# Kernel optimization log

Measured on AMD Instinct MI355X. Metric: run time of the kernel, lower is better.

The kernel has to match this reference:

```python
import jax, jax.numpy as jnp
import numpy as np

BLOCK, HALO, HEADS, DH = 8, 4, 4, 32
EPS = 1e-5


def _convT(x, w, p):
    # torch ConvTranspose2d(stride=1, padding=p) == conv with flipped/transposed kernel, padding k-1-p
    k = w.shape[-1]
    w2 = jnp.flip(w, axis=(-2, -1)).transpose(1, 0, 2, 3)  # (Cin,Cout,k,k) -> (Cout,Cin,k,k)
    pad = k - 1 - p
    return jax.lax.conv_general_dilated(x, w2, (1, 1), ((pad, pad), (pad, pad)),
                                        dimension_numbers=('NCHW', 'OIHW', 'NCHW'))


def _bn(x, g, b, m, v):
    s = g * jax.lax.rsqrt(v + EPS)
    return x * s[None, :, None, None] + (b - m * s)[None, :, None, None]


def _rel_to_abs(x):
    # x: [b, l, 2r-1] -> [b, l, r]
    b, l, m = x.shape
    r = (m + 1) // 2
    x = jnp.concatenate([x, jnp.zeros((b, l, 1), x.dtype)], axis=2)
    flat = jnp.concatenate([x.reshape(b, l * (m + 1)), jnp.zeros((b, m - l), x.dtype)], axis=1)
    return flat.reshape(b, l + 1, m)[:, :l, -r:]


def _rel_logits_1d(q, rel_k):
    # q: [b, x, y, d]; rel_k: [2r-1, d] -> [b, x, r, y, r]
    b, x, y, d = q.shape
    r = (rel_k.shape[0] + 1) // 2
    logits = jnp.einsum('bxyd,rd->bxyr', q, rel_k)
    logits = _rel_to_abs(logits.reshape(b * x, y, -1)).reshape(b, x, y, r)
    return jnp.broadcast_to(logits[:, :, None, :, :], (b, x, r, y, r))


def _rel_pos_emb(q, rel_h, rel_w):
    # q: [bb, block*block, dh] (already scaled, per halonet-pytorch)
    bb, n, d = q.shape
    qg = q.reshape(bb, BLOCK, BLOCK, d)
    lw = _rel_logits_1d(qg, rel_w).transpose(0, 1, 3, 2, 4).reshape(bb, n, -1)  # b (x y) (i j)
    lh = _rel_logits_1d(qg.transpose(0, 2, 1, 3), rel_h).transpose(0, 3, 1, 4, 2).reshape(bb, n, -1)  # b (y x) (j i)
    return lw + lh


def _halo_attn(x, to_q, to_kv, to_out_w, to_out_b, rel_h, rel_w):
    B, C, H, W = x.shape
    b, h = BLOCK, HALO
    nh, nw = H // b, W // b
    nblk = nh * nw
    wsz = b + 2 * h
    inner = to_q.shape[1]
    scale = DH ** -0.5
    # queries: non-overlapping blocks -> [B*nblk, b*b, C]
    q_inp = x.reshape(B, C, nh, b, nw, b).transpose(0, 2, 4, 3, 5, 1).reshape(B * nblk, b * b, C)
    # keys/values: overlapping halo windows (F.unfold) -> [B*nblk, wsz*wsz, C]
    pat = jax.lax.conv_general_dilated_patches(x, (wsz, wsz), (b, b), ((h, h), (h, h)))  # [B, C*wsz*wsz, nh, nw]
    kv_inp = pat.reshape(B, C, wsz * wsz, nblk).transpose(0, 3, 2, 1).reshape(B * nblk, wsz * wsz, C)
    q = q_inp @ to_q
    k, v = jnp.split(kv_inp @ to_kv, 2, axis=-1)
    def heads(t):
        return t.reshape(t.shape[0], t.shape[1], HEADS, DH).transpose(0, 2, 1, 3).reshape(-1, t.shape[1], DH)
    q, k, v = heads(q) * scale, heads(k), heads(v)
    sim = jnp.einsum('bid,bjd->bij', q, k) + _rel_pos_emb(q, rel_h, rel_w)  # [B*nblk*HEADS, b*b, wsz*wsz]
    # mask out halo positions that fall into zero padding
    ones = jnp.ones((1, 1, H, W), x.dtype)
    mpat = jax.lax.conv_general_dilated_patches(ones, (wsz, wsz), (b, b), ((h, h), (h, h)))
    mask = mpat.reshape(wsz * wsz, nblk).T > 0  # [nblk, wsz*wsz]
    neg = -jnp.finfo(sim.dtype).max
    sim = jnp.where(mask[None, :, None, None, :],
                    sim.reshape(B, nblk, HEADS, b * b, wsz * wsz), neg)
    attn = jax.nn.softmax(sim, axis=-1).reshape(-1, b * b, wsz * wsz)
    out = jnp.einsum('bij,bjd->bid', attn, v)
    out = out.reshape(B * nblk, HEADS, b * b, DH).transpose(0, 2, 1, 3).reshape(B * nblk, b * b, inner)
    out = out @ to_out_w + to_out_b
    return out.reshape(B, nh, nw, b, b, C).transpose(0, 5, 1, 3, 2, 4).reshape(B, C, H, W)


def setup_inputs() -> dict:
    key = jax.random.key(0)
    ks = jax.random.split(key, 13)
    B, C, H, W = 2, 128, 192, 192
    inner = HEADS * DH
    rel = 2 * (BLOCK + 2 * HALO) - 1  # 31
    n = lambda k, s, sc: jax.random.normal(k, s, jnp.float32) * sc
    return {
        'x': jax.random.normal(ks[0], (B, C, H, W), jnp.float32),
        'conv1_w': n(ks[1], (C, C, 1, 1), 0.1),
        'bn1_g': jnp.ones((C,), jnp.float32), 'bn1_b': jnp.zeros((C,), jnp.float32),
        'bn1_m': n(ks[2], (C,), 0.1),
        'bn1_v': jax.random.uniform(ks[3], (C,), jnp.float32, 0.5, 1.5),
        'to_q': n(ks[4], (C, inner), 0.05), 'to_kv': n(ks[5], (C, 2 * inner), 0.05),
        'to_out_w': n(ks[6], (inner, C), 0.05), 'to_out_b': n(ks[7], (C,), 0.01),
        'rel_h': n(ks[8], (rel, DH), DH ** -0.5), 'rel_w': n(ks[9], (rel, DH), DH ** -0.5),
        'conv3_w': n(ks[10], (C, C, 3, 3), 0.05),
        'bn3_g': jnp.ones((C,), jnp.float32), 'bn3_b': jnp.zeros((C,), jnp.float32),
        'bn3_m': n(ks[11], (C,), 0.1),
        'bn3_v': jax.random.uniform(ks[12], (C,), jnp.float32, 0.5, 1.5),
    }


def reference(x, conv1_w, bn1_g, bn1_b, bn1_m, bn1_v, to_q, to_kv, to_out_w, to_out_b,
              rel_h, rel_w, conv3_w, bn3_g, bn3_b, bn3_m, bn3_v):
    # Bottleneck (stride=1, no downsample): conv1x1T -> BN -> ReLU -> HaloAttention -> ReLU
    #   -> conv3x3T -> BN -> +identity -> ReLU
    out = jax.nn.relu(_bn(_convT(x, conv1_w, 0), bn1_g, bn1_b, bn1_m, bn1_v))
    out = jax.nn.relu(_halo_attn(out, to_q, to_kv, to_out_w, to_out_b, rel_h, rel_w))
    out = _bn(_convT(out, conv3_w, 1), bn3_g, bn3_b, bn3_m, bn3_v)
    return jax.nn.relu(out + x)
```

## Files before the change

### kernel.cpp

```cpp
#include <hip/hip_runtime.h>
#include <hip/hip_bf16.h>

using bf16 = __hip_bfloat16;
typedef unsigned short u16;
typedef unsigned int   u32;
typedef __attribute__((ext_vector_type(8))) short short8;
typedef __attribute__((ext_vector_type(4))) float f32x4;

#define B_N 2
#define CCH 128
#define HH 192
#define WW 192
#define HWS (HH*WW)
#define NBLKS 576
#define EPSV 1e-5f
#define LDW 136

__device__ __forceinline__ float b2f(bf16 v){ return __bfloat162float(v); }
__device__ __forceinline__ bf16  f2b(float v){ return __float2bfloat16(v); }
__device__ __forceinline__ u32 pck(float a, float b){
    bf16 x = f2b(a), y = f2b(b);
    return (u32)*(u16*)&x | ((u32)*(u16*)&y << 16);
}

__global__ __launch_bounds__(256) void prep_w(
    const float* __restrict__ w1, const float* __restrict__ to_q,
    const float* __restrict__ to_kv, const float* __restrict__ to_ow,
    const float* __restrict__ w3, const float* __restrict__ relh,
    const float* __restrict__ relw, bf16* __restrict__ wb)
{
    int i = blockIdx.x*256 + threadIdx.x;
    float v;
    if (i < 16384){       int co=(i>>7)&127, ci=i&127;      v = w1[ci*128+co]; }
    else if (i < 32768){  int r=i-16384; int co=r>>7, ci=r&127; v = to_q[ci*128+co]*0.17677669529663687f; }
    else if (i < 49152){  int r=i-32768; int co=r>>7, ci=r&127; v = to_kv[ci*256+co]; }
    else if (i < 65536){  int r=i-49152; int co=r>>7, ci=r&127; v = to_kv[ci*256+128+co]; }
    else if (i < 81920){  int r=i-65536; int co=r>>7, ci=r&127; v = to_ow[ci*128+co]; }
    else if (i < 229376){ int r=i-81920; int tap=r>>14, co=(r>>7)&127, ci=r&127; int a=tap/3, b=tap-a*3;
                          v = w3[((size_t)(ci*128+co)*3+a)*3+b]; }
    else if (i < 230400){ int j=i-229376; v = (j < 992) ? relh[j] : 0.f; }
    else                { int j=i-230400; v = (j < 992) ? relw[j] : 0.f; }
    wb[i] = f2b(v);
}

__global__ __launch_bounds__(256) void conv1_mfma(
    const float* __restrict__ x, const bf16* __restrict__ Wp,
    bf16* __restrict__ outp,
    const float* __restrict__ bn_g, const float* __restrict__ bn_b,
    const float* __restrict__ bn_m, const float* __restrict__ bn_v)
{
    __shared__ float tF[128*68];
    __shared__ u16   sX[64*LDW];
    u16* sW = (u16*)tF;
    const int tid  = threadIdx.x;
    const int pix0 = blockIdx.x * 64;
    const int n    = pix0 / HWS;
    const int hwb  = pix0 - n*HWS;
    const int lane = tid & 63;
    const int ln = lane & 15, g = lane >> 4;
    const int cow = (tid >> 6) * 32;

    #pragma unroll
    for (int r = 0; r < 8; ++r){
        int e = tid + r*256;
        int ci = e >> 4, p4 = e & 15;
        *(float4*)&tF[ci*68 + p4*4] =
            *(const float4*)&x[(size_t)(n*CCH + ci)*HWS + hwb + p4*4];
    }
    __syncthreads();
    {
        const int pix = tid & 63, cq = tid >> 6;
        u32 pkt[16];
        #pragma unroll
        for (int c = 0; c < 16; ++c){
            int ci = cq*32 + c*2;
            pkt[c] = pck(tF[ci*68 + pix], tF[(ci+1)*68 + pix]);
        }
        u32* dst = (u32*)&sX[pix*LDW + cq*32];
        #pragma unroll
        for (int c = 0; c < 16; ++c) dst[c] = pkt[c];
    }
    __syncthreads();
    #pragma unroll
    for (int r = 0; r < 8; ++r){
        int e = tid + r*256; int row = e>>4, grp = e&15;
        *(uint4*)&sW[row*LDW + grp*8] = *(const uint4*)&Wp[row*128 + grp*8];
    }
    __syncthreads();

    f32x4 acc[4][2];
    #pragma unroll
    for (int mi=0;mi<4;mi++)
        #pragma unroll
        for (int ni=0;ni<2;ni++) acc[mi][ni] = (f32x4){0.f,0.f,0.f,0.f};
    #pragma unroll
    for (int kk = 0; kk < 4; ++kk){
        short8 fa[4], fb[2];
        #pragma unroll
        for (int mi=0;mi<4;mi++)
            fa[mi] = *(const short8*)&sX[(mi*16+ln)*LDW + kk*32 + g*8];
        #pragma unroll
        for (int ni=0;ni<2;ni++)
            fb[ni] = *(const short8*)&sW[(cow+ni*16+ln)*LDW + kk*32 + g*8];
        #pragma unroll
        for (int mi=0;mi<4;mi++)
            #pragma unroll
            for (int ni=0;ni<2;ni++)
                acc[mi][ni] = __builtin_amdgcn_mfma_f32_16x16x32_bf16(fa[mi], fb[ni], acc[mi][ni], 0, 0, 0);
    }
    float sc[2], bb[2];
    #pragma unroll
    for (int ni=0;ni<2;ni++){
        int co = cow + ni*16 + ln;
        float sg = bn_g[co]*rsqrtf(bn_v[co]+EPSV);
        sc[ni] = sg; bb[ni] = bn_b[co] - bn_m[co]*sg;
    }
    #pragma unroll
    for (int mi=0;mi<4;mi++)
        #pragma unroll
        for (int ni=0;ni<2;ni++)
            #pragma unroll
            for (int j=0;j<4;j++){
                int pix = pix0 + mi*16 + g*4 + j;
                int co  = cow + ni*16 + ln;
                float v = fmaxf(acc[mi][ni][j]*sc[ni] + bb[ni], 0.f);
                outp[(size_t)pix*CCH + co] = f2b(v);
            }
}

template<bool DO_BIAS, bool DO_RELU, bool TRANS_Y2>
__global__ __launch_bounds__(256) void gemm_mfma(
    const bf16* __restrict__ inp, const bf16* __restrict__ Wp,
    bf16* __restrict__ outp, bf16* __restrict__ outp2, int cstride, int choff,
    const float* __restrict__ bias)
{
    Wp    += (size_t)blockIdx.y * 16384;
    choff += blockIdx.y * 128;
    __shared__ u16 sW[128*LDW];
    __shared__ u16 sX[64*LDW];
    const int tid  = threadIdx.x;
    const int pix0 = blockIdx.x * 64;
    const int lane = tid & 63;
    const int ln = lane & 15, g = lane >> 4;
    const int cow = (tid >> 6) * 32;

    #pragma unroll
    for (int r = 0; r < 8; ++r){
        int e = tid + r*256; int row = e>>4, grp = e&15;
        *(uint4*)&sW[row*LDW + grp*8] = *(const uint4*)&Wp[row*128 + grp*8];
    }
    #pragma unroll
    for (int r = 0; r < 4; ++r){
        int e = tid + r*256; int row = e>>4, grp = e&15;
        *(uint4*)&sX[row*LDW + grp*8] = *(const uint4*)&inp[(size_t)(pix0+row)*CCH + grp*8];
    }
    __syncthreads();

    f32x4 acc[4][2];
    #pragma unroll
    for (int mi=0;mi<4;mi++)
        #pragma unroll
        for (int ni=0;ni<2;ni++) acc[mi][ni] = (f32x4){0.f,0.f,0.f,0.f};

    #pragma unroll
    for (int kk = 0; kk < 4; ++kk){
        short8 fa[4], fb[2];
        #pragma unroll
        for (int mi=0;mi<4;mi++)
            fa[mi] = *(const short8*)&sX[(mi*16+ln)*LDW + kk*32 + g*8];
        #pragma unroll
        for (int ni=0;ni<2;ni++)
            fb[ni] = *(const short8*)&sW[(cow+ni*16+ln)*LDW + kk*32 + g*8];
        #pragma unroll
        for (int mi=0;mi<4;mi++)
            #pragma unroll
            for (int ni=0;ni<2;ni++)
                acc[mi][ni] = __builtin_amdgcn_mfma_f32_16x16x32_bf16(fa[mi], fb[ni], acc[mi][ni], 0, 0, 0);
    }

    if (TRANS_Y2 && blockIdx.y == 2){
        __syncthreads();
        u16* tile = sX;
        #pragma unroll
        for (int mi=0;mi<4;mi++)
            #pragma unroll
            for (int ni=0;ni<2;ni++){
                int co   = cow + ni*16 + ln;
                int pixl = mi*16 + g*4;
                *(u32*)&tile[co*68 + pixl]     = pck(acc[mi][ni][0], acc[mi][ni][1]);
                *(u32*)&tile[co*68 + pixl + 2] = pck(acc[mi][ni][2], acc[mi][ni][3]);
            }
        __syncthreads();
        const int co2 = tid >> 1, hf = tid & 1;
        const int n2 = pix0 / HWS, hwb2 = pix0 - n2*HWS;
        u16* gdst = (u16*)outp2 + (size_t)(n2*CCH + co2)*HWS + hwb2 + hf*32;
        const u16* src = &tile[co2*68 + hf*32];
        #pragma unroll
        for (int k=0;k<8;k++)
            *(uint2*)&gdst[k*4] = *(const uint2*)&src[k*4];
        return;
    }

    float bb[2];
    #pragma unroll
    for (int ni=0;ni<2;ni++){
        int co = cow + ni*16 + ln;
        bb[ni] = DO_BIAS ? bias[co] : 0.f;
    }
    #pragma unroll
    for (int mi=0;mi<4;mi++)
        #pragma unroll
        for (int ni=0;ni<2;ni++)
            #pragma unroll
            for (int j=0;j<4;j++){
                int pix = pix0 + mi*16 + g*4 + j;
                int co  = cow + ni*16 + ln;
                float v = acc[mi][ni][j] + bb[ni];
                if (DO_RELU) v = fmaxf(v, 0.f);
                outp[(size_t)pix*cstride + choff + co] = f2b(v);
            }
}

__global__ __launch_bounds__(256) void conv3_mfma(
    const bf16* __restrict__ inp, const bf16* __restrict__ W3p,
    const float* __restrict__ xin, float* __restrict__ outp,
    const float* __restrict__ g3, const float* __restrict__ b3,
    const float* __restrict__ m3, const float* __restrict__ v3)
{
    __shared__ u16 sW[64*136];
    __shared__ u16 sXh[66*136];
    const int tid  = threadIdx.x;
    const int bid  = blockIdx.x;
    const int half = (bid >= 1152) ? 1 : 0;
    const int P0   = (bid - half*1152) * 64;
    const int co0  = half * 64;
    const int n    = P0 / HWS;
    const int hwb  = P0 - n*HWS;
    const int h = hwb / WW, wb = hwb - h*WW;
    const int lane = tid & 63, ln = lane & 15, g = lane >> 4;
    const int w = tid >> 6;

    f32x4 acc[4];
    #pragma unroll
    for (int ni=0;ni<4;ni++) acc[ni] = (f32x4){0.f,0.f,0.f,0.f};

    for (int a = 0; a < 3; ++a){
        const int hs = h + 1 - a;
        if (hs < 0 || hs >= HH) continue;
        const int tap0 = a*3;
        __syncthreads();
        #pragma unroll
        for (int r = 0; r < 5; ++r){
            int e = tid + r*256;
            if (e < 1056){
                int cs = e >> 4, grp = e & 15;
                int col = wb - 1 + cs;
                uint4 val = {0u,0u,0u,0u};
                if (col >= 0 && col < WW)
                    val = *(const uint4*)&inp[(size_t)(n*HWS + hs*WW + col)*CCH + grp*8];
                *(uint4*)&sXh[cs*136 + grp*8] = val;
            }
        }
        #pragma unroll
        for (int r = 0; r < 4; ++r){
            int e = tid + r*256; int row = e>>4, grp = e&15;
            *(uint4*)&sW[row*136 + grp*8] =
                *(const uint4*)&W3p[(size_t)tap0*16384 + (co0+row)*128 + grp*8];
        }
        __syncthreads();
        #pragma unroll
        for (int kk=0;kk<4;++kk){
            short8 fa = *(const short8*)&sW[(w*16+ln)*136 + kk*32 + g*8];
            #pragma unroll
            for (int ni=0;ni<4;++ni){
                short8 fb = *(const short8*)&sXh[(ni*16+ln+2)*136 + kk*32 + g*8];
                acc[ni] = __builtin_amdgcn_mfma_f32_16x16x32_bf16(fa, fb, acc[ni], 0, 0, 0);
            }
        }
        __syncthreads();
        #pragma unroll
        for (int r = 0; r < 4; ++r){
            int e = tid + r*256; int row = e>>4, grp = e&15;
            *(uint4*)&sW[row*136 + grp*8] =
                *(const uint4*)&W3p[(size_t)(tap0+1)*16384 + (co0+row)*128 + grp*8];
        }
        __syncthreads();
        #pragma unroll
        for (int kk=0;kk<4;++kk){
            short8 fa = *(const short8*)&sW[(w*16+ln)*136 + kk*32 + g*8];
            #pragma unroll
            for (int ni=0;ni<4;++ni){
                short8 fb = *(const short8*)&sXh[(ni*16+ln+1)*136 + kk*32 + g*8];
                acc[ni] = __builtin_amdgcn_mfma_f32_16x16x32_bf16(fa, fb, acc[ni], 0, 0, 0);
            }
        }
        __syncthreads();
        #pragma unroll
        for (int r = 0; r < 4; ++r){
            int e = tid + r*256; int row = e>>4, grp = e&15;
            *(uint4*)&sW[row*136 + grp*8] =
                *(const uint4*)&W3p[(size_t)(tap0+2)*16384 + (co0+row)*128 + grp*8];
        }
        __syncthreads();
        #pragma unroll
        for (int kk=0;kk<4;++kk){
            short8 fa = *(const short8*)&sW[(w*16+ln)*136 + kk*32 + g*8];
            #pragma unroll
            for (int ni=0;ni<4;++ni){
                short8 fb = *(const short8*)&sXh[(ni*16+ln)*136 + kk*32 + g*8];
                acc[ni] = __builtin_amdgcn_mfma_f32_16x16x32_bf16(fa, fb, acc[ni], 0, 0, 0);
            }
        }
    }

    #pragma unroll
    for (int j=0;j<4;++j){
        int co = co0 + w*16 + g*4 + j;
        float sg = g3[co]*rsqrtf(v3[co]+EPSV);
        float bc = b3[co] - m3[co]*sg;
        #pragma unroll
        for (int ni=0;ni<4;++ni){
            int pixl = hwb + ni*16 + ln;
            size_t idx = (size_t)(n*CCH + co)*HWS + pixl;
            float v = acc[ni][j]*sg + bc + xin[idx];
            outp[idx] = fmaxf(v, 0.f);
        }
    }
}

__global__ __launch_bounds__(512) void attn_kernel(
    const u16* __restrict__ QK, const u16* __restrict__ vT,
    const u16* __restrict__ relb, bf16* __restrict__ outp)
{
    __shared__ __align__(16) char smem[46848];
    u16*   sK   = (u16*)(smem);
    u16*   sP   = (u16*)(smem);
    u16*   sVT  = (u16*)(smem + 20480);
    float* tT   = (float*)(smem + 37376);
    float* wredM= (float*)(smem + 45824);
    float* wredS= (float*)(smem + 46336);

    const int tid  = threadIdx.x;
    const int bid0 = blockIdx.x;
    const int bid  = (bid0 & 7) * 576 + (bid0 >> 3);
    const int head = bid & 3;
    const int t    = bid >> 2;
    const int n    = t / NBLKS;
    const int blk  = t - n*NBLKS;
    const int bi = blk / 24, bj = blk - bi*24;
    const int row0 = bi*8 - 4, col0 = bj*8 - 4;
    const int ch0 = head*32;
    const int wv = tid >> 6, lane = tid & 63, ln = lane & 15, g = lane >> 4;
    const int nt = wv & 3, mh = wv >> 2;

    uint2 vreg[4];
    #pragma unroll
    for (int r = 0; r < 4; ++r){
        int e = tid + r*512;
        int d   = e >> 6;
        int rem = e & 63;
        int iw  = rem >> 2;
        int jc  = (rem & 3) * 4;
        int rr  = row0 + iw, cc0 = col0 + jc;
        uint2 vv = {0u,0u};
        if (rr >= 0 && rr < HH && cc0 >= 0 && cc0 < 189)
            vv = *(const uint2*)&vT[(size_t)(n*CCH + ch0 + d)*HWS + rr*WW + cc0];
        vreg[r] = vv;
    }

    #pragma unroll
    for (int r = 0; r < 2; ++r){
        int e = tid + r*512;
        int wp = e >> 2, q4 = e & 3;
        int rr = row0 + (wp>>4), cc2 = col0 + (wp&15);
        uint4 kk4 = {0u,0u,0u,0u};
        if (rr>=0 && rr<HH && cc2>=0 && cc2<WW){
            size_t P = (size_t)n*HWS + rr*WW + cc2;
            kk4 = *(const uint4*)&QK[P*256 + 128 + ch0 + q4*8];
        }
        *(uint4*)&sK[wp*40 + q4*8] = kk4;
    }

    const int qc = nt*16 + ln;
    size_t Pq = (size_t)n*HWS + (bi*8 + (qc>>3))*WW + bj*8 + (qc&7);
    const short8 qfrag = *(const short8*)&QK[Pq*256 + ch0 + g*8];
    __syncthreads();

    f32x4 accs[8];
    #pragma unroll
    for (int i=0;i<8;i++){
        short8 fk = *(const short8*)&sK[((mh*8+i)*16+ln)*40 + g*8];
        accs[i] = __builtin_amdgcn_mfma_f32_16x16x32_bf16(fk, qfrag, (f32x4){0.f,0.f,0.f,0.f}, 0, 0, 0);
    }

    {
        const u16* relX = relb + (mh ? 1024 : 0);
        #pragma unroll
        for (int ntr=0; ntr<2; ++ntr){
            short8 fr = *(const short8*)&relX[(ntr*16+ln)*32 + g*8];
            f32x4 L = __builtin_amdgcn_mfma_f32_16x16x32_bf16(qfrag, fr, (f32x4){0.f,0.f,0.f,0.f}, 0, 0, 0);
            #pragma unroll
            for (int r2=0;r2<4;r2++){
                int q  = nt*16 + g*4 + r2;
                int rr = ntr*16 + ln;
                int bq = mh ? (q&7) : (q>>3);
                int iw = rr - 15 + bq;
                if (iw >= 0 && iw < 16) tT[mh*1056 + iw*66 + q] = L[r2];
            }
        }
    }
    __syncthreads();

    float tw[4];
    bool cok[4];
    #pragma unroll
    for (int r2=0;r2<4;r2++){
        tw[r2] = tT[1056 + (g*4+r2)*66 + qc];
        int cc2 = col0 + g*4 + r2;
        cok[r2] = (cc2 >= 0 && cc2 < WW);
    }
    float mx = -3.4e38f;
    #pragma unroll
    for (int i=0;i<8;i++){
        int mt = mh*8 + i;
        int rr = row0 + mt;
        bool rok = (rr >= 0 && rr < HH);
        float th = tT[mt*66 + qc];
        #pragma unroll
        for (int r2=0;r2<4;r2++){
            float s = (rok && cok[r2]) ? (accs[i][r2] + th + tw[r2]) : -3.0e38f;
            accs[i][r2] = s;
            mx = fmaxf(mx, s);
        }
    }
    mx = fmaxf(mx, __shfl_xor(mx, 16));
    mx = fmaxf(mx, __shfl_xor(mx, 32));
    if (g == 0) wredM[mh*64 + qc] = mx;
    __syncthreads();

    #pragma unroll
    for (int r = 0; r < 4; ++r){
        int e = tid + r*512;
        int d   = e >> 6;
        int rem = e & 63;
        int iw  = rem >> 2;
        int jc  = (rem & 3) * 4;
        *(uint2*)&sVT[d*264 + iw*16 + jc] = vreg[r];
    }
    mx = fmaxf(wredM[qc], wredM[64 + qc]);

    float sm = 0.f;
    #pragma unroll
    for (int i=0;i<8;i++){
        #pragma unroll
        for (int r2=0;r2<4;r2++){
            float p = __expf(accs[i][r2] - mx);
            accs[i][r2] = p;
            sm += p;
        }
    }
    sm += __shfl_xor(sm, 16);
    sm += __shfl_xor(sm, 32);
    if (g == 0) wredS[mh*64 + qc] = sm;
    if (mh == 0){
        #pragma unroll
        for (int i=0;i<8;i++){
            u32* dst = (u32*)&sP[qc*136 + i*16 + g*4];
            dst[0] = pck(accs[i][0], accs[i][1]);
            dst[1] = pck(accs[i][2], accs[i][3]);
        }
    }
    __syncthreads();

    const int dt = wv & 1, qt = wv >> 1;
    f32x4 acco = (f32x4){0.f,0.f,0.f,0.f};
    #pragma unroll
    for (int ks=0; ks<4; ++ks){
        short8 fa = *(const short8*)&sVT[(dt*16+ln)*264 + ks*32 + g*8];
        short8 fb = *(const short8*)&sP [(qt*16+ln)*136 + ks*32 + g*8];
        acco = __builtin_amdgcn_mfma_f32_16x16x32_bf16(fa, fb, acco, 0, 0, 0);
    }
    __syncthreads();
    if (mh == 1){
        #pragma unroll
        for (int i=0;i<8;i++){
            u32* dst = (u32*)&sP[qc*136 + i*16 + g*4];
            dst[0] = pck(accs[i][0], accs[i][1]);
            dst[1] = pck(accs[i][2], accs[i][3]);
        }
    }
    __syncthreads();

    #pragma unroll
    for (int ks=0; ks<4; ++ks){
        short8 fa = *(const short8*)&sVT[(dt*16+ln)*264 + 128 + ks*32 + g*8];
        short8 fb = *(const short8*)&sP [(qt*16+ln)*136 + ks*32 + g*8];
        acco = __builtin_amdgcn_mfma_f32_16x16x32_bf16(fa, fb, acco, 0, 0, 0);
    }
    {
        const int q = qt*16 + ln;
        const float inv = 1.f / (wredS[q] + wredS[64 + q]);
        size_t P = (size_t)n*HWS + (bi*8 + (q>>3))*WW + bj*8 + (q&7);
        uint2 ov;
        ov.x = pck(acco[0]*inv, acco[1]*inv);
        ov.y = pck(acco[2]*inv, acco[3]*inv);
        *(uint2*)&outp[P*CCH + ch0 + dt*16 + g*4] = ov;
    }
}

extern "C" void kernel_launch(void* const* d_in, const int* in_sizes, int n_in,
                              void* d_out, int out_size, void* d_ws, size_t ws_size,
                              hipStream_t stream)
{
    (void)in_sizes; (void)n_in; (void)out_size; (void)ws_size;
    const float* x      = (const float*)d_in[0];
    const float* w1     = (const float*)d_in[1];
    const float* bn1_g  = (const float*)d_in[2];
    const float* bn1_b  = (const float*)d_in[3];
    const float* bn1_m  = (const float*)d_in[4];
    const float* bn1_v  = (const float*)d_in[5];
    const float* to_q   = (const float*)d_in[6];
    const float* to_kv  = (const float*)d_in[7];
    const float* to_ow  = (const float*)d_in[8];
    const float* to_ob  = (const float*)d_in[9];
    const float* rel_h  = (const float*)d_in[10];
    const float* rel_w  = (const float*)d_in[11];
    const float* w3     = (const float*)d_in[12];
    const float* bn3_g  = (const float*)d_in[13];
    const float* bn3_b  = (const float*)d_in[14];
    const float* bn3_m  = (const float*)d_in[15];
    const float* bn3_v  = (const float*)d_in[16];

    char* ws   = (char*)d_ws;
    bf16* out1 = (bf16*)(ws + 0);
    bf16* qk   = (bf16*)(ws + 18874368);
    bf16* vT   = (bf16*)(ws + 75497472);
    bf16* wb   = (bf16*)(ws + 94371840);
    bf16* W3p  = wb + 81920;
    u16*  relb = (u16*)(wb + 229376);
    bf16* attnout = (bf16*)d_out;
    bf16* out2    = out1;

    prep_w<<<904, 256, 0, stream>>>(w1, to_q, to_kv, to_ow, w3, rel_h, rel_w, wb);

    conv1_mfma<<<1152, 256, 0, stream>>>(x, wb, out1, bn1_g, bn1_b, bn1_m, bn1_v);
    gemm_mfma<false,false,true><<<dim3(1152,3), 256, 0, stream>>>(
        out1, wb + 16384, qk, vT, 256, 0, nullptr);

    attn_kernel<<<4608, 512, 0, stream>>>((const u16*)qk, (const u16*)vT,
                                          relb, attnout);

    gemm_mfma<true,true,false><<<dim3(1152,1), 256, 0, stream>>>(
        attnout, wb + 65536, out2, nullptr, 128, 0, to_ob);

    conv3_mfma<<<2304, 256, 0, stream>>>(out2, W3p, x, (float*)d_out,
                                         bn3_g, bn3_b, bn3_m, bn3_v);
}
```

Baseline: 156.3 us.

## Shrink attention LDS footprint and add interior fast path without bounds checks

Cuts the attention kernel's shared memory in three ways. The K and V^T LDS row strides are narrowed (40→36 and 264→260), and the relative-position logit table is stored as bf16 instead of fp32. This is meant to let more 512-thread blocks fit per CU. Interior blocks, whose halo window is fully in bounds, also get separate load and masking paths that skip the per-element bounds checks. The risks are misaligned 16-byte LDS accesses from the new strides, possible bank conflicts, and slightly less accurate positional logits.

```diff
diff --git a/kernel.cpp b/kernel.cpp
--- a/kernel.cpp
+++ b/kernel.cpp
@@ -332,13 +332,13 @@
     const u16* __restrict__ QK, const u16* __restrict__ vT,
     const u16* __restrict__ relb, bf16* __restrict__ outp)
 {
-    __shared__ __align__(16) char smem[46848];
+    __shared__ __align__(16) char smem[40320];
     u16*   sK   = (u16*)(smem);
     u16*   sP   = (u16*)(smem);
-    u16*   sVT  = (u16*)(smem + 20480);
-    float* tT   = (float*)(smem + 37376);
-    float* wredM= (float*)(smem + 45824);
-    float* wredS= (float*)(smem + 46336);
+    u16*   sVT  = (u16*)(smem + 18432);
+    u16*   tT   = (u16*)(smem + 35072);
+    float* wredM= (float*)(smem + 39296);
+    float* wredS= (float*)(smem + 39808);
 
     const int tid  = threadIdx.x;
     const int bid0 = blockIdx.x;
@@ -352,33 +352,53 @@
     const int ch0 = head*32;
     const int wv = tid >> 6, lane = tid & 63, ln = lane & 15, g = lane >> 4;
     const int nt = wv & 3, mh = wv >> 2;
+    const bool interior = (bi >= 1) && (bi <= 22) && (bj >= 1) && (bj <= 22);
 
     uint2 vreg[4];
-    #pragma unroll
-    for (int r = 0; r < 4; ++r){
-        int e = tid + r*512;
-        int d   = e >> 6;
-        int rem = e & 63;
-        int iw  = rem >> 2;
-        int jc  = (rem & 3) * 4;
-        int rr  = row0 + iw, cc0 = col0 + jc;
-        uint2 vv = {0u,0u};
-        if (rr >= 0 && rr < HH && cc0 >= 0 && cc0 < 189)
-            vv = *(const uint2*)&vT[(size_t)(n*CCH + ch0 + d)*HWS + rr*WW + cc0];
-        vreg[r] = vv;
-    }
-
-    #pragma unroll
-    for (int r = 0; r < 2; ++r){
-        int e = tid + r*512;
-        int wp = e >> 2, q4 = e & 3;
-        int rr = row0 + (wp>>4), cc2 = col0 + (wp&15);
-        uint4 kk4 = {0u,0u,0u,0u};
-        if (rr>=0 && rr<HH && cc2>=0 && cc2<WW){
-            size_t P = (size_t)n*HWS + rr*WW + cc2;
-            kk4 = *(const uint4*)&QK[P*256 + 128 + ch0 + q4*8];
-        }
-        *(uint4*)&sK[wp*40 + q4*8] = kk4;
+    if (interior){
+        #pragma unroll
+        for (int r = 0; r < 4; ++r){
+            int e = tid + r*512;
+            int d = e >> 6, rem = e & 63;
+            int iw = rem >> 2, jc = (rem & 3) * 4;
+            vreg[r] = *(const uint2*)&vT[(size_t)(n*CCH + ch0 + d)*HWS
+                                         + (row0+iw)*WW + col0 + jc];
+        }
+    } else {
+        #pragma unroll
+        for (int r = 0; r < 4; ++r){
+            int e = tid + r*512;
+            int d = e >> 6, rem = e & 63;
+            int iw = rem >> 2, jc = (rem & 3) * 4;
+            int rr = row0 + iw, cc0 = col0 + jc;
+            uint2 vv = {0u,0u};
+            if (rr >= 0 && rr < HH && cc0 >= 0 && cc0 < 189)
+                vv = *(const uint2*)&vT[(size_t)(n*CCH + ch0 + d)*HWS + rr*WW + cc0];
+            vreg[r] = vv;
+        }
+    }
+
+    if (interior){
+        #pragma unroll
+        for (int r = 0; r < 2; ++r){
+            int e = tid + r*512;
+            int wp = e >> 2, q4 = e & 3;
+            size_t P = (size_t)n*HWS + (row0 + (wp>>4))*WW + col0 + (wp&15);
+            *(uint4*)&sK[wp*36 + q4*8] = *(const uint4*)&QK[P*256 + 128 + ch0 + q4*8];
+        }
+    } else {
+        #pragma unroll
+        for (int r = 0; r < 2; ++r){
+            int e = tid + r*512;
+            int wp = e >> 2, q4 = e & 3;
+            int rr = row0 + (wp>>4), cc2 = col0 + (wp&15);
+            uint4 kk4 = {0u,0u,0u,0u};
+            if (rr>=0 && rr<HH && cc2>=0 && cc2<WW){
+                size_t P = (size_t)n*HWS + rr*WW + cc2;
+                kk4 = *(const uint4*)&QK[P*256 + 128 + ch0 + q4*8];
+            }
+            *(uint4*)&sK[wp*36 + q4*8] = kk4;
+        }
     }
 
     const int qc = nt*16 + ln;
@@ -389,7 +409,7 @@
     f32x4 accs[8];
     #pragma unroll
     for (int i=0;i<8;i++){
-        short8 fk = *(const short8*)&sK[((mh*8+i)*16+ln)*40 + g*8];
+        short8 fk = *(const short8*)&sK[((mh*8+i)*16+ln)*36 + g*8];
         accs[i] = __builtin_amdgcn_mfma_f32_16x16x32_bf16(fk, qfrag, (f32x4){0.f,0.f,0.f,0.f}, 0, 0, 0);
     }
 
@@ -405,32 +425,50 @@
                 int rr = ntr*16 + ln;
                 int bq = mh ? (q&7) : (q>>3);
                 int iw = rr - 15 + bq;
-                if (iw >= 0 && iw < 16) tT[mh*1056 + iw*66 + q] = L[r2];
+                if (iw >= 0 && iw < 16){
+                    bf16 tb16 = f2b(L[r2]);
+                    tT[mh*1056 + iw*66 + q] = *(u16*)&tb16;
+                }
             }
         }
     }
     __syncthreads();
 
     float tw[4];
-    bool cok[4];
-    #pragma unroll
-    for (int r2=0;r2<4;r2++){
-        tw[r2] = tT[1056 + (g*4+r2)*66 + qc];
-        int cc2 = col0 + g*4 + r2;
-        cok[r2] = (cc2 >= 0 && cc2 < WW);
-    }
+    #pragma unroll
+    for (int r2=0;r2<4;r2++)
+        tw[r2] = b2f(*(bf16*)&tT[1056 + (g*4+r2)*66 + qc]);
     float mx = -3.4e38f;
-    #pragma unroll
-    for (int i=0;i<8;i++){
-        int mt = mh*8 + i;
-        int rr = row0 + mt;
-        bool rok = (rr >= 0 && rr < HH);
-        float th = tT[mt*66 + qc];
+    if (interior){
+        #pragma unroll
+        for (int i=0;i<8;i++){
+            float th = b2f(*(bf16*)&tT[(mh*8+i)*66 + qc]);
+            #pragma unroll
+            for (int r2=0;r2<4;r2++){
+                float s = accs[i][r2] + th + tw[r2];
+                accs[i][r2] = s;
+                mx = fmaxf(mx, s);
+            }
+        }
+    } else {
+        bool cok[4];
         #pragma unroll
         for (int r2=0;r2<4;r2++){
-            float s = (rok && cok[r2]) ? (accs[i][r2] + th + tw[r2]) : -3.0e38f;
-            accs[i][r2] = s;
-            mx = fmaxf(mx, s);
+            int cc2 = col0 + g*4 + r2;
+            cok[r2] = (cc2 >= 0 && cc2 < WW);
+        }
+        #pragma unroll
+        for (int i=0;i<8;i++){
+            int mt = mh*8 + i;
+            int rr = row0 + mt;
+            bool rok = (rr >= 0 && rr < HH);
+            float th = b2f(*(bf16*)&tT[mt*66 + qc]);
+            #pragma unroll
+            for (int r2=0;r2<4;r2++){
+                float s = (rok && cok[r2]) ? (accs[i][r2] + th + tw[r2]) : -3.0e38f;
+                accs[i][r2] = s;
+                mx = fmaxf(mx, s);
+            }
         }
     }
     mx = fmaxf(mx, __shfl_xor(mx, 16));
@@ -441,11 +479,9 @@
     #pragma unroll
     for (int r = 0; r < 4; ++r){
         int e = tid + r*512;
-        int d   = e >> 6;
-        int rem = e & 63;
-        int iw  = rem >> 2;
-        int jc  = (rem & 3) * 4;
-        *(uint2*)&sVT[d*264 + iw*16 + jc] = vreg[r];
+        int d = e >> 6, rem = e & 63;
+        int iw = rem >> 2, jc = (rem & 3) * 4;
+        *(uint2*)&sVT[d*260 + iw*16 + jc] = vreg[r];
     }
     mx = fmaxf(wredM[qc], wredM[64 + qc]);
 
@@ -476,7 +512,7 @@
     f32x4 acco = (f32x4){0.f,0.f,0.f,0.f};
     #pragma unroll
     for (int ks=0; ks<4; ++ks){
-        short8 fa = *(const short8*)&sVT[(dt*16+ln)*264 + ks*32 + g*8];
+        short8 fa = *(const short8*)&sVT[(dt*16+ln)*260 + ks*32 + g*8];
         short8 fb = *(const short8*)&sP [(qt*16+ln)*136 + ks*32 + g*8];
         acco = __builtin_amdgcn_mfma_f32_16x16x32_bf16(fa, fb, acco, 0, 0, 0);
     }
@@ -493,7 +529,7 @@
 
     #pragma unroll
     for (int ks=0; ks<4; ++ks){
-        short8 fa = *(const short8*)&sVT[(dt*16+ln)*264 + 128 + ks*32 + g*8];
+        short8 fa = *(const short8*)&sVT[(dt*16+ln)*260 + 128 + ks*32 + g*8];
         short8 fb = *(const short8*)&sP [(qt*16+ln)*136 + ks*32 + g*8];
         acco = __builtin_amdgcn_mfma_f32_16x16x32_bf16(fa, fb, acco, 0, 0, 0);
     }
```

After: 213.8 us. 36.7% more time.
